# Optimization experiments

Measured on AMD Instinct MI355X. Metric: run time of the kernel, lower is better.

Reference implementation:

```python
import jax, jax.numpy as jnp
import numpy as np

B, M, N = 8, 512, 1024
D_TS, D_LLM, H, E = 1024, 4096, 16, 64
NEG_INF = float('-inf')


def setup_inputs() -> dict:
    key = jax.random.key(0)
    ks = jax.random.split(key, 12)
    s = 0.02
    return {
        'ts': jax.random.normal(ks[0], (B, M, D_TS), jnp.float32),
        'kv': jax.random.normal(ks[1], (B, N, D_LLM), jnp.float32),
        'ts_mask': jax.random.randint(ks[2], (B, M, 1), 0, 2).astype(jnp.float32),
        'kv_mask': jax.random.randint(ks[3], (B, 1, 1, N), 0, 2).astype(jnp.bool_),
        'Wq': jax.random.normal(ks[4], (D_TS, H * E), jnp.float32) * s,
        'bq': jnp.zeros((H * E,), jnp.float32),
        'Wk': jax.random.normal(ks[5], (D_LLM, H * E), jnp.float32) * s,
        'bk': jnp.zeros((H * E,), jnp.float32),
        'Wv': jax.random.normal(ks[6], (D_LLM, H * E), jnp.float32) * s,
        'bv': jnp.zeros((H * E,), jnp.float32),
        'Wo': jax.random.normal(ks[7], (H * E, D_LLM), jnp.float32) * s,
        'bo': jnp.zeros((D_LLM,), jnp.float32),
    }


def reference(ts, kv, ts_mask, kv_mask, Wq, bq, Wk, bk, Wv, bv, Wo, bo):
    b, m, _ = ts.shape
    n = kv.shape[-2]
    q = (ts @ Wq + bq).reshape(b, m, H, E)   # (B,M,H,E)
    k = (kv @ Wk + bk).reshape(b, n, H, E)   # (B,N,H,E)
    v = (kv @ Wv + bv).reshape(b, n, H, E)
    scores = jnp.einsum('bmhe,bnhe->bhmn', q, k) * (1.0 / np.sqrt(E))
    # masked_fill: True in kv_mask -> -inf
    scores = jnp.where(kv_mask, NEG_INF, scores)
    A = jax.nn.softmax(scores, axis=-1)  # dropout is identity in eval
    out_v = jnp.einsum('bhmn,bnhe->bmhe', A, v).reshape(b, m, H * E)
    out = (out_v @ Wo + bo) * ts_mask
    valid = (ts_mask != 0)[..., 0]  # (B,M)
    scores_for_log = jnp.where(~valid[:, None, :, None], NEG_INF, scores)
    return out, scores_for_log
```

## Files before the change

kernel.cpp:

```cpp
#include <hip/hip_runtime.h>
#include <math.h>

namespace {
constexpr int B_   = 8;
constexpr int M_   = 512;
constexpr int N_   = 1024;
constexpr int DTS  = 1024;
constexpr int DLLM = 4096;
constexpr int H_   = 16;
constexpr int E_   = 64;
constexpr int HE   = H_ * E_;
constexpr float NEG_BIG = -3.0e38f;
}

typedef __attribute__((ext_vector_type(4))) float f32x4;
typedef __attribute__((ext_vector_type(8))) short short8;
typedef unsigned int uint;
typedef unsigned short ushort;

__device__ inline void bsplit(float x, ushort& h, ushort& l) {
  uint u = __float_as_uint(x);
  uint hr = (u + 0x7FFFu + ((u >> 16) & 1u)) & 0xFFFF0000u;
  float lof = x - __uint_as_float(hr);
  h = (ushort)(hr >> 16);
  l = (ushort)(__float_as_uint(lof) >> 16);
}
__device__ inline uint pk(ushort a, ushort b) { return (uint)a | ((uint)b << 16); }

__device__ inline void gld16(const void* g, void* l) {
  __builtin_amdgcn_global_load_lds(
      (const __attribute__((address_space(1))) uint*)g,
      (__attribute__((address_space(3))) uint*)l, 16, 0, 0);
}

__global__ __launch_bounds__(256) void asplit_kernel(
    const float* __restrict__ X, ushort* __restrict__ Xh,
    ushort* __restrict__ Xl, int n8) {
  const int idx = blockIdx.x * 256 + threadIdx.x;
  if (idx >= n8) return;
  const float4 a = *(const float4*)(X + (size_t)idx * 8);
  const float4 b = *(const float4*)(X + (size_t)idx * 8 + 4);
  float f[8] = {a.x, a.y, a.z, a.w, b.x, b.y, b.z, b.w};
  short8 h, l;
#pragma unroll
  for (int j = 0; j < 8; ++j) {
    ushort hh, ll;
    bsplit(f[j], hh, ll);
    h[j] = (short)hh;
    l[j] = (short)ll;
  }
  *(short8*)(Xh + (size_t)idx * 8) = h;
  *(short8*)(Xl + (size_t)idx * 8) = l;
}

__global__ __launch_bounds__(256) void tsplit_kernel(
    const float* __restrict__ W, ushort* __restrict__ Wth,
    ushort* __restrict__ Wtl, int K, int Nc) {
  __shared__ float S[32][33];
  const int t = threadIdx.x;
  const int n0 = blockIdx.x * 32, k0 = blockIdx.y * 32;
  const int c = t & 31, r8 = t >> 5;
#pragma unroll
  for (int i = 0; i < 4; ++i) {
    const int rr = r8 + i * 8;
    S[rr][c] = W[(size_t)(k0 + rr) * Nc + n0 + c];
  }
  __syncthreads();
#pragma unroll
  for (int i = 0; i < 4; ++i) {
    const int nn = r8 + i * 8;
    const float x = S[c][nn];
    ushort h, l;
    bsplit(x, h, l);
    const size_t o = (size_t)(n0 + nn) * K + k0 + c;
    Wth[o] = h;
    Wtl[o] = l;
  }
}

__global__ __launch_bounds__(256) void vtprep_kernel(
    const float* __restrict__ V, ushort* __restrict__ Vth,
    ushort* __restrict__ Vtl) {
  __shared__ float S[64][68];
  const int t  = threadIdx.x;
  const int nt = blockIdx.x & 15;
  const int h  = (blockIdx.x >> 4) & 15;
  const int b  = blockIdx.x >> 8;
  const int n0 = nt * 64;
#pragma unroll
  for (int i = 0; i < 4; ++i) {
    const int idx = i * 256 + t;
    const int row = idx >> 4, c4 = (idx & 15) * 4;
    *(float4*)&S[row][c4] =
        *(const float4*)&V[(size_t)(b * N_ + n0 + row) * HE + h * 64 + c4];
  }
  __syncthreads();
  const int e = t >> 2, nch = (t & 3) * 16;
  short8 h0, h1, l0, l1;
#pragma unroll
  for (int j = 0; j < 8; ++j) {
    ushort hh, ll;
    bsplit(S[nch + j][e], hh, ll);
    h0[j] = (short)hh; l0[j] = (short)ll;
    bsplit(S[nch + 8 + j][e], hh, ll);
    h1[j] = (short)hh; l1[j] = (short)ll;
  }
  const size_t off = (size_t)((b * H_ + h) * 64 + e) * N_ + n0 + nch;
  *(short8*)(Vth + off)     = h0;
  *(short8*)(Vth + off + 8) = h1;
  *(short8*)(Vtl + off)     = l0;
  *(short8*)(Vtl + off + 8) = l1;
}

template <bool ROWMASK, bool SPLITOUT>
__global__ __launch_bounds__(256) void gemm_split3_kernel(
    const float* __restrict__ A, const ushort* __restrict__ Bth,
    const ushort* __restrict__ Btl, const float* __restrict__ bias,
    const float* __restrict__ rowmask, float* __restrict__ C,
    ushort* __restrict__ Ch, ushort* __restrict__ Cl, int Kd, int Nc) {
  __shared__ ushort Ah[128][32];
  __shared__ ushort Al[128][32];
  __shared__ ushort Bh[128][32];
  __shared__ ushort Bl[128][32];

  const int t    = threadIdx.x;
  const int lane = t & 63;
  const int wv   = t >> 6;
  const int l15  = lane & 15;
  const int quad = lane >> 4;
  const int wm   = (wv & 1) * 64;
  const int wn   = (wv >> 1) * 64;
  const int row0 = blockIdx.y * 128;
  const int col0 = blockIdx.x * 128;

  const int arow = t >> 1;
  const int half = t & 1;
  const float* Ap = A + (size_t)(row0 + arow) * Kd + half * 16;

  const int bn  = (lane >> 2);
  const int bk8 = (lane & 3) * 8;
  const ushort* Bhp = Bth + (size_t)(col0 + wv * 32 + bn) * Kd + bk8;
  const ushort* Blp = Btl + (size_t)(col0 + wv * 32 + bn) * Kd + bk8;

  f32x4 acc[4][4];
#pragma unroll
  for (int i = 0; i < 4; ++i)
#pragma unroll
    for (int j = 0; j < 4; ++j) acc[i][j] = {0.f, 0.f, 0.f, 0.f};

  for (int k0 = 0; k0 < Kd; k0 += 32) {
    __syncthreads();
#pragma unroll
    for (int j = 0; j < 2; ++j) {
      const int n = wv * 32 + j * 16 + bn;
      gld16(Bhp + (size_t)j * 16 * Kd + k0, &Bh[n][bk8]);
      gld16(Blp + (size_t)j * 16 * Kd + k0, &Bl[n][bk8]);
    }
    float f[16];
#pragma unroll
    for (int i = 0; i < 4; ++i) {
      const float4 v = *(const float4*)(Ap + k0 + i * 4);
      f[i * 4 + 0] = v.x; f[i * 4 + 1] = v.y;
      f[i * 4 + 2] = v.z; f[i * 4 + 3] = v.w;
    }
    ushort hh[16], ll[16];
#pragma unroll
    for (int i = 0; i < 16; ++i) bsplit(f[i], hh[i], ll[i]);
    uint4 wh0 = {pk(hh[0], hh[1]), pk(hh[2], hh[3]), pk(hh[4], hh[5]), pk(hh[6], hh[7])};
    uint4 wh1 = {pk(hh[8], hh[9]), pk(hh[10], hh[11]), pk(hh[12], hh[13]), pk(hh[14], hh[15])};
    uint4 wl0 = {pk(ll[0], ll[1]), pk(ll[2], ll[3]), pk(ll[4], ll[5]), pk(ll[6], ll[7])};
    uint4 wl1 = {pk(ll[8], ll[9]), pk(ll[10], ll[11]), pk(ll[12], ll[13]), pk(ll[14], ll[15])};
    *(uint4*)&Ah[arow][half * 16 + 0] = wh0;
    *(uint4*)&Ah[arow][half * 16 + 8] = wh1;
    *(uint4*)&Al[arow][half * 16 + 0] = wl0;
    *(uint4*)&Al[arow][half * 16 + 8] = wl1;

    __syncthreads();

    short8 ah[4], al[4], bh[4], bl[4];
#pragma unroll
    for (int mi = 0; mi < 4; ++mi) {
      ah[mi] = *(const short8*)&Ah[wm + mi * 16 + l15][quad * 8];
      al[mi] = *(const short8*)&Al[wm + mi * 16 + l15][quad * 8];
    }
#pragma unroll
    for (int ni = 0; ni < 4; ++ni) {
      bh[ni] = *(const short8*)&Bh[wn + ni * 16 + l15][quad * 8];
      bl[ni] = *(const short8*)&Bl[wn + ni * 16 + l15][quad * 8];
    }
#pragma unroll
    for (int mi = 0; mi < 4; ++mi)
#pragma unroll
      for (int ni = 0; ni < 4; ++ni) {
        acc[mi][ni] = __builtin_amdgcn_mfma_f32_16x16x32_bf16(
            ah[mi], bh[ni], acc[mi][ni], 0, 0, 0);
        acc[mi][ni] = __builtin_amdgcn_mfma_f32_16x16x32_bf16(
            ah[mi], bl[ni], acc[mi][ni], 0, 0, 0);
        acc[mi][ni] = __builtin_amdgcn_mfma_f32_16x16x32_bf16(
            al[mi], bh[ni], acc[mi][ni], 0, 0, 0);
      }
  }

  float bb[4];
#pragma unroll
  for (int ni = 0; ni < 4; ++ni) bb[ni] = bias[col0 + wn + ni * 16 + l15];
#pragma unroll
  for (int mi = 0; mi < 4; ++mi)
#pragma unroll
    for (int r = 0; r < 4; ++r) {
      const int row = row0 + wm + mi * 16 + quad * 4 + r;
      const float rm = ROWMASK ? rowmask[row] : 1.f;
#pragma unroll
      for (int ni = 0; ni < 4; ++ni) {
        const int col = col0 + wn + ni * 16 + l15;
        float v = acc[mi][ni][r] + bb[ni];
        if (SPLITOUT) {
          ushort vh, vl;
          bsplit(v, vh, vl);
          Ch[(size_t)row * Nc + col] = vh;
          Cl[(size_t)row * Nc + col] = vl;
        } else {
          if (ROWMASK) v *= rm;
          C[(size_t)row * Nc + col] = v;
        }
      }
    }
}

template <bool ROWMASK, bool SPLITOUT>
__global__ __launch_bounds__(256) void gemm_bb_kernel(
    const ushort* __restrict__ Ath, const ushort* __restrict__ Atl,
    const ushort* __restrict__ Bth, const ushort* __restrict__ Btl,
    const float* __restrict__ bias, const float* __restrict__ rowmask,
    float* __restrict__ C, ushort* __restrict__ Ch, ushort* __restrict__ Cl,
    int Kd, int Nc) {
  __shared__ ushort Ah[128][32];
  __shared__ ushort Al[128][32];
  __shared__ ushort Bh[128][32];
  __shared__ ushort Bl[128][32];

  const int t    = threadIdx.x;
  const int lane = t & 63;
  const int wv   = t >> 6;
  const int l15  = lane & 15;
  const int quad = lane >> 4;
  const int wm   = (wv & 1) * 64;
  const int wn   = (wv >> 1) * 64;
  const int row0 = blockIdx.y * 128;
  const int col0 = blockIdx.x * 128;

  const int rn  = (lane >> 2);
  const int rk8 = (lane & 3) * 8;
  const ushort* Ahp = Ath + (size_t)(row0 + wv * 32 + rn) * Kd + rk8;
  const ushort* Alp = Atl + (size_t)(row0 + wv * 32 + rn) * Kd + rk8;
  const ushort* Bhp = Bth + (size_t)(col0 + wv * 32 + rn) * Kd + rk8;
  const ushort* Blp = Btl + (size_t)(col0 + wv * 32 + rn) * Kd + rk8;

  f32x4 acc[4][4];
#pragma unroll
  for (int i = 0; i < 4; ++i)
#pragma unroll
    for (int j = 0; j < 4; ++j) acc[i][j] = {0.f, 0.f, 0.f, 0.f};

  for (int k0 = 0; k0 < Kd; k0 += 32) {
    __syncthreads();
#pragma unroll
    for (int j = 0; j < 2; ++j) {
      const int rr = wv * 32 + j * 16 + rn;
      gld16(Ahp + (size_t)j * 16 * Kd + k0, &Ah[rr][rk8]);
      gld16(Alp + (size_t)j * 16 * Kd + k0, &Al[rr][rk8]);
      gld16(Bhp + (size_t)j * 16 * Kd + k0, &Bh[rr][rk8]);
      gld16(Blp + (size_t)j * 16 * Kd + k0, &Bl[rr][rk8]);
    }
    __syncthreads();

    short8 ah[4], al[4], bh[4], bl[4];
#pragma unroll
    for (int mi = 0; mi < 4; ++mi) {
      ah[mi] = *(const short8*)&Ah[wm + mi * 16 + l15][quad * 8];
      al[mi] = *(const short8*)&Al[wm + mi * 16 + l15][quad * 8];
    }
#pragma unroll
    for (int ni = 0; ni < 4; ++ni) {
      bh[ni] = *(const short8*)&Bh[wn + ni * 16 + l15][quad * 8];
      bl[ni] = *(const short8*)&Bl[wn + ni * 16 + l15][quad * 8];
    }
#pragma unroll
    for (int mi = 0; mi < 4; ++mi)
#pragma unroll
      for (int ni = 0; ni < 4; ++ni) {
        acc[mi][ni] = __builtin_amdgcn_mfma_f32_16x16x32_bf16(
            ah[mi], bh[ni], acc[mi][ni], 0, 0, 0);
        acc[mi][ni] = __builtin_amdgcn_mfma_f32_16x16x32_bf16(
            ah[mi], bl[ni], acc[mi][ni], 0, 0, 0);
        acc[mi][ni] = __builtin_amdgcn_mfma_f32_16x16x32_bf16(
            al[mi], bh[ni], acc[mi][ni], 0, 0, 0);
      }
  }

  float bb[4];
#pragma unroll
  for (int ni = 0; ni < 4; ++ni) bb[ni] = bias[col0 + wn + ni * 16 + l15];
#pragma unroll
  for (int mi = 0; mi < 4; ++mi)
#pragma unroll
    for (int r = 0; r < 4; ++r) {
      const int row = row0 + wm + mi * 16 + quad * 4 + r;
      const float rm = ROWMASK ? rowmask[row] : 1.f;
#pragma unroll
      for (int ni = 0; ni < 4; ++ni) {
        const int col = col0 + wn + ni * 16 + l15;
        float v = acc[mi][ni][r] + bb[ni];
        if (SPLITOUT) {
          ushort vh, vl;
          bsplit(v, vh, vl);
          Ch[(size_t)row * Nc + col] = vh;
          Cl[(size_t)row * Nc + col] = vl;
        } else {
          if (ROWMASK) v *= rm;
          C[(size_t)row * Nc + col] = v;
        }
      }
    }
}

__global__ __launch_bounds__(256) void attn_mfma_kernel(
    const ushort* __restrict__ Qh, const ushort* __restrict__ Ql,
    const ushort* __restrict__ Kh, const ushort* __restrict__ Kl,
    const ushort* __restrict__ Vth, const ushort* __restrict__ Vtl,
    const unsigned char* __restrict__ kvmask, const float* __restrict__ tsmask,
    float* __restrict__ outv, float* __restrict__ scores_out) {
  __shared__ __align__(16) ushort sm[24576];
  ushort* KHT = sm;
  ushort* KLT = sm + 4096;
  ushort* VTH = sm + 8192;
  ushort* VTL = sm + 12288;
  ushort* QHT = sm + 16384;
  ushort* QLT = sm + 20480;

  const int t = threadIdx.x, lane = t & 63, wv = t >> 6;
  const int l15 = lane & 15, quad = lane >> 4;
  const int blk = blockIdx.x;
  const int mt = blk & 7;
  const int h  = (blk >> 3) & 15;
  const int b  = blk >> 7;
  const int m0 = mt * 64;
  const int lrow = lane >> 3, lch = lane & 7;
  const int gch8 = (lch ^ (lrow & 7)) * 8;

#pragma unroll
  for (int i = 0; i < 2; ++i) {
    const int rr = wv * 16 + i * 8;
    const size_t g = (size_t)(b * M_ + m0 + rr + lrow) * HE + h * 64 + gch8;
    gld16(Qh + g, &QHT[rr * 64]);
    gld16(Ql + g, &QLT[rr * 64]);
  }
  __syncthreads();

  short8 qh[2], ql[2];
#pragma unroll
  for (int ks = 0; ks < 2; ++ks) {
    const int row = wv * 16 + l15;
    const int off = row * 64 + (((ks * 4 + quad) ^ (row & 7)) << 3);
    qh[ks] = *(const short8*)&QHT[off];
    ql[ks] = *(const short8*)&QLT[off];
  }
  __builtin_amdgcn_s_waitcnt(0);

  uint* Pu = (uint*)(sm + 16384) + wv * 1024;

  float tsm_v[4];
#pragma unroll
  for (int r = 0; r < 4; ++r)
    tsm_v[r] = tsmask[b * M_ + m0 + wv * 16 + quad * 4 + r];

  float m_i[4] = {-INFINITY, -INFINITY, -INFINITY, -INFINITY};
  float l_i[4] = {0.f, 0.f, 0.f, 0.f};
  f32x4 acc[4];
#pragma unroll
  for (int es = 0; es < 4; ++es) acc[es] = {0.f, 0.f, 0.f, 0.f};

  for (int nc = 0; nc < 16; ++nc) {
    const int n0 = nc * 64;
    __syncthreads();
#pragma unroll
    for (int i = 0; i < 2; ++i) {
      const int rr = wv * 16 + i * 8;
      const size_t gk = (size_t)(b * N_ + n0 + rr + lrow) * HE + h * 64 + gch8;
      const size_t gv = (size_t)((b * H_ + h) * 64 + rr + lrow) * N_ + n0 + gch8;
      gld16(Kh + gk, &KHT[rr * 64]);
      gld16(Kl + gk, &KLT[rr * 64]);
      gld16(Vth + gv, &VTH[rr * 64]);
      gld16(Vtl + gv, &VTL[rr * 64]);
    }
    __syncthreads();

    f32x4 s[4];
#pragma unroll
    for (int ns = 0; ns < 4; ++ns) {
      s[ns] = {0.f, 0.f, 0.f, 0.f};
#pragma unroll
      for (int ks = 0; ks < 2; ++ks) {
        const int row = ns * 16 + l15;
        const int off = row * 64 + (((ks * 4 + quad) ^ (row & 7)) << 3);
        const short8 kh = *(const short8*)&KHT[off];
        const short8 kl = *(const short8*)&KLT[off];
        s[ns] = __builtin_amdgcn_mfma_f32_16x16x32_bf16(qh[ks], kh, s[ns], 0, 0, 0);
        s[ns] = __builtin_amdgcn_mfma_f32_16x16x32_bf16(qh[ks], kl, s[ns], 0, 0, 0);
        s[ns] = __builtin_amdgcn_mfma_f32_16x16x32_bf16(ql[ks], kh, s[ns], 0, 0, 0);
      }
    }

    bool km[4];
#pragma unroll
    for (int ns = 0; ns < 4; ++ns)
      km[ns] = kvmask[b * N_ + n0 + ns * 16 + l15] != 0;
    float sc[4][4];
#pragma unroll
    for (int ns = 0; ns < 4; ++ns)
#pragma unroll
      for (int r = 0; r < 4; ++r)
        sc[r][ns] = km[ns] ? -INFINITY : s[ns][r] * 0.125f;

#pragma unroll
    for (int r = 0; r < 4; ++r) {
      const size_t base =
          ((size_t)(b * H_ + h) * M_ + m0 + wv * 16 + quad * 4 + r) * N_ + n0;
      const bool vr = tsm_v[r] != 0.f;
#pragma unroll
      for (int ns = 0; ns < 4; ++ns)
        scores_out[base + ns * 16 + l15] =
            (vr && !km[ns]) ? sc[r][ns] : NEG_BIG;
    }

#pragma unroll
    for (int r = 0; r < 4; ++r) {
      float cm = fmaxf(fmaxf(sc[r][0], sc[r][1]), fmaxf(sc[r][2], sc[r][3]));
#pragma unroll
      for (int o = 1; o < 16; o <<= 1) cm = fmaxf(cm, __shfl_xor(cm, o));
      const float nm = fmaxf(m_i[r], cm);
      const float alpha = (m_i[r] == -INFINITY) ? 0.f : __expf(m_i[r] - nm);
      float ps = 0.f;
      const int pr = quad * 4 + r;
#pragma unroll
      for (int ns = 0; ns < 4; ++ns) {
        const float p = (sc[r][ns] == -INFINITY) ? 0.f : __expf(sc[r][ns] - nm);
        ps += p;
        ushort ph_, pl_;
        bsplit(p, ph_, pl_);
        const int c = ns * 16 + l15;
        Pu[pr * 64 + (((c >> 2) ^ (pr & 7)) << 2) + (c & 3)] = pk(ph_, pl_);
      }
#pragma unroll
      for (int o = 1; o < 16; o <<= 1) ps += __shfl_xor(ps, o);
      l_i[r] = l_i[r] * alpha + ps;
      m_i[r] = nm;
#pragma unroll
      for (int es = 0; es < 4; ++es) acc[es][r] *= alpha;
    }

#pragma unroll
    for (int ks = 0; ks < 2; ++ks) {
      const int c0 = ks * 8 + quad * 2;
      const uint* pb = &Pu[l15 * 64];
      const uint4 u0 = *(const uint4*)&pb[(c0 ^ (l15 & 7)) << 2];
      const uint4 u1 = *(const uint4*)&pb[((c0 + 1) ^ (l15 & 7)) << 2];
      short8 ph, pl;
      const uint* up0 = (const uint*)&u0;
      const uint* up1 = (const uint*)&u1;
#pragma unroll
      for (int j = 0; j < 4; ++j) {
        ph[j] = (short)(up0[j] & 0xffffu); pl[j] = (short)(up0[j] >> 16);
        ph[4 + j] = (short)(up1[j] & 0xffffu); pl[4 + j] = (short)(up1[j] >> 16);
      }
#pragma unroll
      for (int es = 0; es < 4; ++es) {
        const int row = es * 16 + l15;
        const int off = row * 64 + (((ks * 4 + quad) ^ (row & 7)) << 3);
        const short8 vh = *(const short8*)&VTH[off];
        const short8 vl = *(const short8*)&VTL[off];
        acc[es] = __builtin_amdgcn_mfma_f32_16x16x32_bf16(ph, vh, acc[es], 0, 0, 0);
        acc[es] = __builtin_amdgcn_mfma_f32_16x16x32_bf16(ph, vl, acc[es], 0, 0, 0);
        acc[es] = __builtin_amdgcn_mfma_f32_16x16x32_bf16(pl, vh, acc[es], 0, 0, 0);
      }
    }
  }

#pragma unroll
  for (int r = 0; r < 4; ++r) {
    const float inv = (l_i[r] > 0.f) ? 1.f / l_i[r] : 0.f;
    const int grow = b * M_ + m0 + wv * 16 + quad * 4 + r;
#pragma unroll
    for (int es = 0; es < 4; ++es)
      outv[(size_t)grow * HE + h * 64 + es * 16 + l15] = acc[es][r] * inv;
  }
}

extern "C" void kernel_launch(void* const* d_in, const int* in_sizes, int n_in,
                              void* d_out, int out_size, void* d_ws,
                              size_t ws_size, hipStream_t stream) {
  const float* ts  = (const float*)d_in[0];
  const float* kv  = (const float*)d_in[1];
  const float* tsm = (const float*)d_in[2];
  const unsigned char* kvm = (const unsigned char*)d_in[3];
  const float* Wq = (const float*)d_in[4];
  const float* bq = (const float*)d_in[5];
  const float* Wk = (const float*)d_in[6];
  const float* bk = (const float*)d_in[7];
  const float* Wv = (const float*)d_in[8];
  const float* bv = (const float*)d_in[9];
  const float* Wo = (const float*)d_in[10];
  const float* bo = (const float*)d_in[11];

  float* out        = (float*)d_out;
  float* scores_out = out + (size_t)B_ * M_ * DLLM;

  char* ws = (char*)d_ws;
  constexpr size_t MB = 1024 * 1024;

  if (ws_size >= 260 * MB) {
    ushort* Kvh  = (ushort*)(ws);
    ushort* Kvl  = (ushort*)(ws + 64 * MB);
    float*  Vf   = (float*)(ws + 128 * MB);
    ushort* Khp  = (ushort*)(ws + 160 * MB);
    ushort* Klp  = (ushort*)(ws + 176 * MB);
    ushort* Qhp  = (ushort*)(ws + 192 * MB);
    ushort* Qlp  = (ushort*)(ws + 200 * MB);
    ushort* Tsh  = (ushort*)(ws + 208 * MB);
    ushort* Tsl  = (ushort*)(ws + 216 * MB);
    ushort* Wqh  = (ushort*)(ws + 224 * MB);
    ushort* Wql  = (ushort*)(ws + 226 * MB);
    ushort* Wkh  = (ushort*)(ws + 228 * MB);
    ushort* Wkl  = (ushort*)(ws + 236 * MB);
    ushort* Wvh  = (ushort*)(ws + 244 * MB);
    ushort* Wvl  = (ushort*)(ws + 252 * MB);
    ushort* Vthp  = (ushort*)(ws);
    ushort* Vtlp  = (ushort*)(ws + 16 * MB);
    ushort* outvh = (ushort*)(ws + 32 * MB);
    ushort* outvl = (ushort*)(ws + 40 * MB);
    ushort* Woh   = (ushort*)(ws + 64 * MB);
    ushort* Wol   = (ushort*)(ws + 72 * MB);
    float*  outv  = (float*)(ws + 128 * MB);

    {
      const int n8_ts = (B_ * M_ * DTS) / 8;
      asplit_kernel<<<dim3(n8_ts / 256), 256, 0, stream>>>(ts, Tsh, Tsl, n8_ts);
      const int n8_kv = (B_ * N_ * DLLM) / 8;
      asplit_kernel<<<dim3(n8_kv / 256), 256, 0, stream>>>(kv, Kvh, Kvl, n8_kv);
    }

    tsplit_kernel<<<dim3(HE / 32, DTS / 32), 256, 0, stream>>>(Wq, Wqh, Wql, DTS, HE);
    tsplit_kernel<<<dim3(HE / 32, DLLM / 32), 256, 0, stream>>>(Wk, Wkh, Wkl, DLLM, HE);
    tsplit_kernel<<<dim3(HE / 32, DLLM / 32), 256, 0, stream>>>(Wv, Wvh, Wvl, DLLM, HE);

    gemm_bb_kernel<false, true><<<dim3(HE / 128, (B_ * M_) / 128), 256, 0, stream>>>(
        Tsh, Tsl, Wqh, Wql, bq, nullptr, nullptr, Qhp, Qlp, DTS, HE);
    gemm_bb_kernel<false, true><<<dim3(HE / 128, (B_ * N_) / 128), 256, 0, stream>>>(
        Kvh, Kvl, Wkh, Wkl, bk, nullptr, nullptr, Khp, Klp, DLLM, HE);
    gemm_bb_kernel<false, false><<<dim3(HE / 128, (B_ * N_) / 128), 256, 0, stream>>>(
        Kvh, Kvl, Wvh, Wvl, bv, nullptr, Vf, nullptr, nullptr, DLLM, HE);

    vtprep_kernel<<<dim3(B_ * H_ * 16), 256, 0, stream>>>(Vf, Vthp, Vtlp);

    attn_mfma_kernel<<<dim3(B_ * H_ * (M_ / 64)), 256, 0, stream>>>(
        Qhp, Qlp, Khp, Klp, Vthp, Vtlp, kvm, tsm, outv, scores_out);

    {
      const int n8_o = (B_ * M_ * HE) / 8;
      asplit_kernel<<<dim3(n8_o / 256), 256, 0, stream>>>(outv, outvh, outvl, n8_o);
    }

    tsplit_kernel<<<dim3(DLLM / 32, HE / 32), 256, 0, stream>>>(Wo, Woh, Wol, HE, DLLM);
    gemm_bb_kernel<true, false><<<dim3(DLLM / 128, (B_ * M_) / 128), 256, 0, stream>>>(
        outvh, outvl, Woh, Wol, bo, tsm, out, nullptr, nullptr, HE, DLLM);
  } else {
    float*  Vf   = (float*)(ws);
    float*  outv = (float*)(ws);
    ushort* Qhp  = (ushort*)(ws + 32 * MB);
    ushort* Qlp  = (ushort*)(ws + 40 * MB);
    ushort* Khp  = (ushort*)(ws + 48 * MB);
    ushort* Klp  = (ushort*)(ws + 64 * MB);
    ushort* Wqh  = (ushort*)(ws + 80 * MB);
    ushort* Wql  = (ushort*)(ws + 82 * MB);
    ushort* Wkh  = (ushort*)(ws + 84 * MB);
    ushort* Wkl  = (ushort*)(ws + 92 * MB);
    ushort* Wvh  = (ushort*)(ws + 100 * MB);
    ushort* Wvl  = (ushort*)(ws + 108 * MB);
    ushort* Vthp = (ushort*)(ws + 84 * MB);
    ushort* Vtlp = (ushort*)(ws + 100 * MB);
    ushort* Woh  = (ushort*)(ws + 48 * MB);
    ushort* Wol  = (ushort*)(ws + 56 * MB);

    tsplit_kernel<<<dim3(HE / 32, DTS / 32), 256, 0, stream>>>(Wq, Wqh, Wql, DTS, HE);
    tsplit_kernel<<<dim3(HE / 32, DLLM / 32), 256, 0, stream>>>(Wk, Wkh, Wkl, DLLM, HE);
    tsplit_kernel<<<dim3(HE / 32, DLLM / 32), 256, 0, stream>>>(Wv, Wvh, Wvl, DLLM, HE);

    gemm_split3_kernel<false, true><<<dim3(HE / 128, (B_ * M_) / 128), 256, 0, stream>>>(
        ts, Wqh, Wql, bq, nullptr, nullptr, Qhp, Qlp, DTS, HE);
    gemm_split3_kernel<false, true><<<dim3(HE / 128, (B_ * N_) / 128), 256, 0, stream>>>(
        kv, Wkh, Wkl, bk, nullptr, nullptr, Khp, Klp, DLLM, HE);
    gemm_split3_kernel<false, false><<<dim3(HE / 128, (B_ * N_) / 128), 256, 0, stream>>>(
        kv, Wvh, Wvl, bv, nullptr, Vf, nullptr, nullptr, DLLM, HE);

    vtprep_kernel<<<dim3(B_ * H_ * 16), 256, 0, stream>>>(Vf, Vthp, Vtlp);

    attn_mfma_kernel<<<dim3(B_ * H_ * (M_ / 64)), 256, 0, stream>>>(
        Qhp, Qlp, Khp, Klp, Vthp, Vtlp, kvm, tsm, outv, scores_out);

    tsplit_kernel<<<dim3(DLLM / 32, HE / 32), 256, 0, stream>>>(Wo, Woh, Wol, HE, DLLM);
    gemm_split3_kernel<true, false><<<dim3(DLLM / 128, (B_ * M_) / 128), 256, 0, stream>>>(
        outv, Woh, Wol, bo, tsm, out, nullptr, nullptr, HE, DLLM);
  }
}
```

Baseline: 1.311 ms.

## Double-buffer LDS tiles and XOR-swizzle chunks in split-bf16 GEMM

The split-bf16 GEMM kernel now keeps two LDS stages per operand. It prefetches the next K-slice while the MFMAs run on the current one, and uses a single barrier per iteration instead of two. The 16-byte chunks are also XOR-swizzled by row, on the global-load side and on the fragment reads, to reduce LDS bank conflicts. This doubles LDS use per block to 64 KB, which may lower occupancy. Correctness relies on the barrier draining the async global-to-LDS loads.

```diff
diff --git a/kernel.cpp b/kernel.cpp
--- a/kernel.cpp
+++ b/kernel.cpp
@@ -234,10 +234,10 @@
     const float* __restrict__ bias, const float* __restrict__ rowmask,
     float* __restrict__ C, ushort* __restrict__ Ch, ushort* __restrict__ Cl,
     int Kd, int Nc) {
-  __shared__ ushort Ah[128][32];
-  __shared__ ushort Al[128][32];
-  __shared__ ushort Bh[128][32];
-  __shared__ ushort Bl[128][32];
+  __shared__ ushort Ah[2][128][32];
+  __shared__ ushort Al[2][128][32];
+  __shared__ ushort Bh[2][128][32];
+  __shared__ ushort Bl[2][128][32];
 
   const int t    = threadIdx.x;
   const int lane = t & 63;
@@ -249,12 +249,14 @@
   const int row0 = blockIdx.y * 128;
   const int col0 = blockIdx.x * 128;
 
-  const int rn  = (lane >> 2);
-  const int rk8 = (lane & 3) * 8;
-  const ushort* Ahp = Ath + (size_t)(row0 + wv * 32 + rn) * Kd + rk8;
-  const ushort* Alp = Atl + (size_t)(row0 + wv * 32 + rn) * Kd + rk8;
-  const ushort* Bhp = Bth + (size_t)(col0 + wv * 32 + rn) * Kd + rk8;
-  const ushort* Blp = Btl + (size_t)(col0 + wv * 32 + rn) * Kd + rk8;
+  const int srow = lane >> 2;
+  const int sch8 = ((lane & 3) ^ (srow & 3)) * 8;
+  const ushort* Ahp = Ath + (size_t)(row0 + wv * 32 + srow) * Kd + sch8;
+  const ushort* Alp = Atl + (size_t)(row0 + wv * 32 + srow) * Kd + sch8;
+  const ushort* Bhp = Bth + (size_t)(col0 + wv * 32 + srow) * Kd + sch8;
+  const ushort* Blp = Btl + (size_t)(col0 + wv * 32 + srow) * Kd + sch8;
+
+  const int fsw = (quad ^ (l15 & 3)) * 8;
 
   f32x4 acc[4][4];
 #pragma unroll
@@ -262,28 +264,44 @@
 #pragma unroll
     for (int j = 0; j < 4; ++j) acc[i][j] = {0.f, 0.f, 0.f, 0.f};
 
+#pragma unroll
+  for (int j = 0; j < 2; ++j) {
+    const int rr = wv * 32 + j * 16;
+    const size_t o = (size_t)j * 16 * Kd;
+    gld16(Ahp + o, &Ah[0][rr][0]);
+    gld16(Alp + o, &Al[0][rr][0]);
+    gld16(Bhp + o, &Bh[0][rr][0]);
+    gld16(Blp + o, &Bl[0][rr][0]);
+  }
+  __syncthreads();
+
+  int cur = 0;
   for (int k0 = 0; k0 < Kd; k0 += 32) {
-    __syncthreads();
-#pragma unroll
-    for (int j = 0; j < 2; ++j) {
-      const int rr = wv * 32 + j * 16 + rn;
-      gld16(Ahp + (size_t)j * 16 * Kd + k0, &Ah[rr][rk8]);
-      gld16(Alp + (size_t)j * 16 * Kd + k0, &Al[rr][rk8]);
-      gld16(Bhp + (size_t)j * 16 * Kd + k0, &Bh[rr][rk8]);
-      gld16(Blp + (size_t)j * 16 * Kd + k0, &Bl[rr][rk8]);
-    }
-    __syncthreads();
+    if (k0 + 32 < Kd) {
+      const int nb = cur ^ 1;
+#pragma unroll
+      for (int j = 0; j < 2; ++j) {
+        const int rr = wv * 32 + j * 16;
+        const size_t o = (size_t)j * 16 * Kd + k0 + 32;
+        gld16(Ahp + o, &Ah[nb][rr][0]);
+        gld16(Alp + o, &Al[nb][rr][0]);
+        gld16(Bhp + o, &Bh[nb][rr][0]);
+        gld16(Blp + o, &Bl[nb][rr][0]);
+      }
+    }
 
     short8 ah[4], al[4], bh[4], bl[4];
 #pragma unroll
     for (int mi = 0; mi < 4; ++mi) {
-      ah[mi] = *(const short8*)&Ah[wm + mi * 16 + l15][quad * 8];
-      al[mi] = *(const short8*)&Al[wm + mi * 16 + l15][quad * 8];
+      const int row = wm + mi * 16 + l15;
+      ah[mi] = *(const short8*)&Ah[cur][row][fsw];
+      al[mi] = *(const short8*)&Al[cur][row][fsw];
     }
 #pragma unroll
     for (int ni = 0; ni < 4; ++ni) {
-      bh[ni] = *(const short8*)&Bh[wn + ni * 16 + l15][quad * 8];
-      bl[ni] = *(const short8*)&Bl[wn + ni * 16 + l15][quad * 8];
+      const int row = wn + ni * 16 + l15;
+      bh[ni] = *(const short8*)&Bh[cur][row][fsw];
+      bl[ni] = *(const short8*)&Bl[cur][row][fsw];
     }
 #pragma unroll
     for (int mi = 0; mi < 4; ++mi)
@@ -296,6 +314,9 @@
         acc[mi][ni] = __builtin_amdgcn_mfma_f32_16x16x32_bf16(
             al[mi], bh[ni], acc[mi][ni], 0, 0, 0);
       }
+
+    __syncthreads();
+    cur ^= 1;
   }
 
   float bb[4];
```

After: 1.333 ms. About the same (+1.6%).
